# Performance work log

Hardware: AMD Instinct MI355X
Metric: run time of the kernel (lower is better)

The kernel has to match this reference:

```python
import jax, jax.numpy as jnp
import numpy as np

N_HEAD = 8
NORM_GROUPS = 32
EPS = 1e-6


def setup_inputs() -> dict:
    key = jax.random.key(0)
    ks = jax.random.split(key, 9)
    B, C, H, W, D = 1, 256, 16, 16, 16
    COND = 512
    x = jax.random.normal(ks[0], (B, C, H, W, D), dtype=jnp.float32)
    cond = jax.random.normal(ks[1], (B, COND), dtype=jnp.float32)
    # AdaGN linear scale/shift (torch Linear: weight [C, cond_dim], bias [C])
    w_scale = jax.random.normal(ks[2], (C, COND), dtype=jnp.float32) * 0.02
    b_scale = jax.random.normal(ks[3], (C,), dtype=jnp.float32) * 0.02
    w_shift = jax.random.normal(ks[4], (C, COND), dtype=jnp.float32) * 0.02
    b_shift = jax.random.normal(ks[5], (C,), dtype=jnp.float32) * 0.02
    # 1x1x1 conv3d weights collapse to matrices: qkv [3C, C] (no bias), out [C, C] + bias
    w_qkv = jax.random.normal(ks[6], (3 * C, C), dtype=jnp.float32) * (1.0 / np.sqrt(C))
    w_out = jax.random.normal(ks[7], (C, C), dtype=jnp.float32) * (1.0 / np.sqrt(C))
    b_out = jax.random.normal(ks[8], (C,), dtype=jnp.float32) * 0.02
    return {"x": x, "cond": cond, "w_scale": w_scale, "b_scale": b_scale,
            "w_shift": w_shift, "b_shift": b_shift, "w_qkv": w_qkv,
            "w_out": w_out, "b_out": b_out}


def _ada_gn(x, cond, w_scale, b_scale, w_shift, b_shift):
    B, C, H, W, D = x.shape
    G = NORM_GROUPS
    xg = x.reshape(B, G, C // G, H, W, D)
    mean = jnp.mean(xg, axis=(2, 3, 4, 5), keepdims=True)
    var = jnp.var(xg, axis=(2, 3, 4, 5), keepdims=True)
    x_norm = ((xg - mean) * jax.lax.rsqrt(var + EPS)).reshape(B, C, H, W, D)
    scale = (cond @ w_scale.T + b_scale)[:, :, None, None, None]  # [B,C,1,1,1]
    shift = (cond @ w_shift.T + b_shift)[:, :, None, None, None]
    return x_norm * (1.0 + scale) + shift


def reference(x, cond, w_scale, b_scale, w_shift, b_shift, w_qkv, w_out, b_out):
    B, C, H, W, D = x.shape
    nh = N_HEAD
    hd = C // nh
    N = H * W * D  # flattened spatial tokens
    norm = _ada_gn(x, cond, w_scale, b_scale, w_shift, b_shift)
    # 1x1x1 conv == channel matmul
    qkv = jnp.einsum('oc,bchwd->bohwd', w_qkv, norm)        # [B,3C,H,W,D]
    qkv = qkv.reshape(B, nh, 3 * hd, N)
    q, k, v = jnp.split(qkv, 3, axis=2)                      # each [B,nh,hd,N]
    attn = jnp.einsum('bnci,bncj->bnij', q, k) / jnp.sqrt(jnp.float32(C))
    attn = jax.nn.softmax(attn, axis=-1)                     # [B,nh,N,N]
    out = jnp.einsum('bnij,bncj->bnci', attn, v)             # [B,nh,hd,N]
    out = out.reshape(B, C, H, W, D)
    out = jnp.einsum('oc,bchwd->bohwd', w_out, out) + b_out[None, :, None, None, None]
    return out + x
```

## Files before the change

kernel.cpp:

```cpp
#include <hip/hip_runtime.h>
#include <math.h>

#define CCH 256
#define NN  4096
#define NHEAD 8
#define CONDD 512

typedef __attribute__((ext_vector_type(8))) short short8;
typedef __attribute__((ext_vector_type(4))) float f32x4;
typedef __attribute__((ext_vector_type(16))) float f32x16;

static __device__ __forceinline__ short f2bf(float f) {
    union { float f; uint32_t u; } v; v.f = f;
    uint32_t r = v.u + 0x7fffu + ((v.u >> 16) & 1u);
    return (short)(r >> 16);
}

static __device__ __forceinline__ uint32_t cvt_pk_bf16(float a, float b) {
    uint32_t r;
    asm("v_cvt_pk_bf16_f32 %0, %1, %2" : "=v"(r) : "v"(a), "v"(b));
    return r;
}

__global__ __launch_bounds__(256) void front_fused(const float* __restrict__ x,
                                                   const float* __restrict__ cond,
                                                   const float* __restrict__ w_scale,
                                                   const float* __restrict__ b_scale,
                                                   const float* __restrict__ w_shift,
                                                   const float* __restrict__ b_shift,
                                                   const float* __restrict__ wq,
                                                   const float* __restrict__ wo,
                                                   float* __restrict__ partial,
                                                   float* __restrict__ scale,
                                                   float* __restrict__ shift,
                                                   short* __restrict__ wqb,
                                                   short* __restrict__ wob) {
    __shared__ float rs[4], rss[4];
    int bb = blockIdx.x;
    int t = threadIdx.x;
    if (bb < 256) {
        const float4* p = (const float4*)(x + bb * 4096);
        float s = 0.f, ss = 0.f;
        for (int k = t; k < 1024; k += 256) {
            float4 v = p[k];
            s += v.x + v.y + v.z + v.w;
            ss += v.x * v.x + v.y * v.y + v.z * v.z + v.w * v.w;
        }
        #pragma unroll
        for (int off = 32; off; off >>= 1) { s += __shfl_xor(s, off); ss += __shfl_xor(ss, off); }
        int wid = t >> 6;
        if ((t & 63) == 0) { rs[wid] = s; rss[wid] = ss; }
        __syncthreads();
        if (t == 0) {
            partial[2 * bb] = rs[0] + rs[1] + rs[2] + rs[3];
            partial[2 * bb + 1] = rss[0] + rss[1] + rss[2] + rss[3];
        }
    } else if (bb < 1280) {
        int idx = (bb - 256) * 256 + t;
        if (idx < 196608) wqb[idx] = f2bf(wq[idx]);
        else              wob[idx - 196608] = f2bf(wo[idx - 196608]);
    } else {
        int o = (bb - 1280) * 4 + (t >> 6);
        int lane = t & 63;
        float ds = 0.f, dh = 0.f;
        for (int k = lane; k < CONDD; k += 64) {
            float cv = cond[k];
            ds += cv * w_scale[o * CONDD + k];
            dh += cv * w_shift[o * CONDD + k];
        }
        #pragma unroll
        for (int off = 32; off; off >>= 1) { ds += __shfl_xor(ds, off); dh += __shfl_xor(dh, off); }
        if (lane == 0) { scale[o] = ds + b_scale[o]; shift[o] = dh + b_shift[o]; }
    }
}

__global__ __launch_bounds__(256) void normalize_t(const float* __restrict__ x,
                                                   const float* __restrict__ partial,
                                                   const float* __restrict__ scale,
                                                   const float* __restrict__ shift,
                                                   short* __restrict__ norm_t) {
    __shared__ float gm[8], gr[8];
    __shared__ float Aa[64], Bb[64];
    __shared__ short tile[32 * 66];
    int i0 = blockIdx.x * 32;
    int c0 = blockIdx.y * 64;
    int g0 = c0 >> 3;
    int t = threadIdx.x;
    if (t < 8) {
        float s = 0.f, ss = 0.f;
        #pragma unroll
        for (int ch = 0; ch < 8; ++ch) {
            s += partial[((g0 + t) * 8 + ch) * 2];
            ss += partial[((g0 + t) * 8 + ch) * 2 + 1];
        }
        float mean = s * (1.0f / 32768.0f);
        float var = ss * (1.0f / 32768.0f) - mean * mean;
        gm[t] = mean;
        gr[t] = rsqrtf(var + 1e-6f);
    }
    __syncthreads();
    if (t < 64) {
        int c = c0 + t;
        float a = gr[t >> 3] * (1.0f + scale[c]);
        Aa[t] = a;
        Bb[t] = shift[c] - gm[t >> 3] * a;
    }
    __syncthreads();
    #pragma unroll
    for (int e0 = 0; e0 < 8; ++e0) {
        int e = e0 * 256 + t;
        int cl = e >> 5, il = e & 31;
        float v = x[(c0 + cl) * NN + i0 + il];
        tile[il * 66 + cl] = f2bf(v * Aa[cl] + Bb[cl]);
    }
    __syncthreads();
    #pragma unroll
    for (int e0 = 0; e0 < 4; ++e0) {
        int e = e0 * 256 + t;
        int il = e >> 5, cd = e & 31;
        uint32_t d = *(const uint32_t*)&tile[il * 66 + 2 * cd];
        *(uint32_t*)&norm_t[(i0 + il) * 256 + c0 + 2 * cd] = d;
    }
}

__global__ __launch_bounds__(256) void qkv_gemm(const short* __restrict__ wqb,
                                                const short* __restrict__ norm_t,
                                                short* __restrict__ qtb, short* __restrict__ ktb,
                                                short* __restrict__ vcb) {
    int t = threadIdx.x;
    int w = t >> 6, lane = t & 63, li = lane & 15, lg = lane >> 4;
    int o0 = blockIdx.x * 32;
    int i0 = blockIdx.y * 64 + w * 16;
    f32x4 acc[2] = {{0,0,0,0},{0,0,0,0}};
    const short* bbase = norm_t + (i0 + li) * 256 + 8 * lg;
    const short* abase = wqb + (o0 + li) * 256 + 8 * lg;
    #pragma unroll
    for (int ks = 0; ks < 8; ++ks) {
        short8 bfrag = *(const short8*)(bbase + ks * 32);
        #pragma unroll
        for (int f = 0; f < 2; ++f) {
            short8 afrag = *(const short8*)(abase + f * 16 * 256 + ks * 32);
            acc[f] = __builtin_amdgcn_mfma_f32_16x16x32_bf16(afrag, bfrag, acc[f], 0, 0, 0);
        }
    }
    int i = i0 + li;
    #pragma unroll
    for (int f = 0; f < 2; ++f) {
        #pragma unroll
        for (int r = 0; r < 4; ++r) {
            int o = o0 + 16 * f + 4 * lg + r;
            float v = acc[f][r];
            int h = o / 96;
            int rr = o - h * 96;
            int cc = rr & 31;
            int kind = rr >> 5;
            if (kind == 0)      qtb[(h * NN + i) * 32 + cc] = f2bf(v * (0.0625f * 1.44269504f));
            else if (kind == 1) ktb[(h * NN + i) * 32 + cc] = f2bf(v);
            else                vcb[(h * 32 + cc) * NN + i] = f2bf(v);
        }
    }
}

__global__ __launch_bounds__(512, 4) void attention_mfma(const short* __restrict__ qtb,
                                                         const short* __restrict__ ktb,
                                                         const short* __restrict__ vcb,
                                                         short* __restrict__ attnP,
                                                         float* __restrict__ plsum) {
    __shared__ __align__(16) char lds[65536];

    int bid = blockIdx.x;
    int h = bid & 7;
    int qb = (bid >> 3) & 15;
    int kh = bid >> 7;
    int t = threadIdx.x;
    int w = t >> 6, lane = t & 63, l31 = lane & 31, hi = lane >> 5;

    int qbase = qb * 256 + w * 32;
    const short* qrow = qtb + (h * NN + qbase + l31) * 32;
    short8 qf0 = *(const short8*)(qrow + 8 * hi);
    short8 qf1 = *(const short8*)(qrow + 16 + 8 * hi);
    asm volatile("s_waitcnt vmcnt(0)" ::: "memory");

    const char* src0;
    const char* src1;
    int ldsoff0, ldsoff1, step;
    if (w < 4) {
        int row_l = lane >> 2, g_lds = lane & 3;
        int g_glob = g_lds ^ (row_l & 3);
        const char* kbase = (const char*)ktb + (size_t)(h * NN + kh * 1024) * 64;
        int s0 = 2 * w, s1 = 2 * w + 1;
        src0 = kbase + ((s0 >> 2) * 64 + (s0 & 3) * 16 + row_l) * 64 + g_glob * 16;
        src1 = kbase + ((s1 >> 2) * 64 + (s1 & 3) * 16 + row_l) * 64 + g_glob * 16;
        ldsoff0 = s0 * 1024;
        ldsoff1 = s1 * 1024;
        step = 8192;
    } else {
        int row_l = lane >> 3, vs_lds = lane & 7;
        int vg = vs_lds ^ row_l;
        const char* vbase = (const char*)vcb + (size_t)(h * 32) * (NN * 2) + kh * 2048;
        int s0 = 2 * (w - 4), s1 = 2 * (w - 4) + 1;
        src0 = vbase + (size_t)((s0 & 3) * 8 + row_l) * (NN * 2) + (s0 >> 2) * 128 + vg * 16;
        src1 = vbase + (size_t)((s1 & 3) * 8 + row_l) * (NN * 2) + (s1 >> 2) * 128 + vg * 16;
        ldsoff0 = 8192 + s0 * 1024;
        ldsoff1 = 8192 + s1 * 1024;
        step = 256;
    }

    f32x16 acc = {0,0,0,0,0,0,0,0,0,0,0,0,0,0,0,0};
    const f32x16 zero16 = {0,0,0,0,0,0,0,0,0,0,0,0,0,0,0,0};
    float lsum = 0.f;

    #define ISSUE(st, b) do { \
        __builtin_amdgcn_global_load_lds((const uint32_t*)(src0 + (st) * step), \
            (uint32_t*)(lds + (b) * 16384 + ldsoff0), 16, 0, 0); \
        __builtin_amdgcn_global_load_lds((const uint32_t*)(src1 + (st) * step), \
            (uint32_t*)(lds + (b) * 16384 + ldsoff1), 16, 0, 0); \
    } while (0)

    #define COMPUTE(b) do { \
        const char* bb_ = lds + (b) * 16384; \
        _Pragma("unroll") \
        for (int chunk = 0; chunk < 2; ++chunk) { \
            _Pragma("unroll") \
            for (int half = 0; half < 2; ++half) { \
                int jl = half * 32; \
                int R = jl + l31; \
                int rx = R & 3; \
                const char* kr = bb_ + chunk * 4096 + R * 64; \
                short8 kf0 = *(const short8*)(kr + (((hi) ^ rx) << 4)); \
                short8 kf1 = *(const short8*)(kr + (((2 + hi) ^ rx) << 4)); \
                const char* vr = bb_ + 8192 + chunk * 4096 + l31 * 128; \
                int cx = l31 & 7; \
                int sv = (jl >> 3) + hi; \
                short8 vf0 = *(const short8*)(vr + ((sv ^ cx) << 4)); \
                short8 vf1 = *(const short8*)(vr + (((sv + 2) ^ cx) << 4)); \
                __builtin_amdgcn_s_setprio(1); \
                f32x16 s = __builtin_amdgcn_mfma_f32_32x32x16_bf16(kf0, qf0, zero16, 0, 0, 0); \
                s = __builtin_amdgcn_mfma_f32_32x32x16_bf16(kf1, qf1, s, 0, 0, 0); \
                __builtin_amdgcn_s_setprio(0); \
                float p[16]; \
                _Pragma("unroll") \
                for (int r = 0; r < 16; ++r) p[r] = __builtin_amdgcn_exp2f(s[r]); \
                float u0 = 0.f, u1 = 0.f; \
                _Pragma("unroll") \
                for (int r = 0; r < 4; ++r) { u0 += p[r] + p[4 + r]; u1 += p[8 + r] + p[12 + r]; } \
                lsum += u0 + u1; \
                auto A1 = __builtin_amdgcn_permlane32_swap(cvt_pk_bf16(p[0], p[1]),   cvt_pk_bf16(p[4], p[5]),   false, false); \
                auto A2 = __builtin_amdgcn_permlane32_swap(cvt_pk_bf16(p[2], p[3]),   cvt_pk_bf16(p[6], p[7]),   false, false); \
                auto A3 = __builtin_amdgcn_permlane32_swap(cvt_pk_bf16(p[8], p[9]),   cvt_pk_bf16(p[12], p[13]), false, false); \
                auto A4 = __builtin_amdgcn_permlane32_swap(cvt_pk_bf16(p[10], p[11]), cvt_pk_bf16(p[14], p[15]), false, false); \
                union PF { uint32_t u[4]; short8 s8; }; \
                PF f1, f2; \
                f1.u[0] = A1[0]; f1.u[1] = A2[0]; f1.u[2] = A1[1]; f1.u[3] = A2[1]; \
                f2.u[0] = A3[0]; f2.u[1] = A4[0]; f2.u[2] = A3[1]; f2.u[3] = A4[1]; \
                __builtin_amdgcn_s_setprio(1); \
                acc = __builtin_amdgcn_mfma_f32_32x32x16_bf16(vf0, f1.s8, acc, 0, 0, 0); \
                acc = __builtin_amdgcn_mfma_f32_32x32x16_bf16(vf1, f2.s8, acc, 0, 0, 0); \
                __builtin_amdgcn_s_setprio(0); \
            } \
        } \
    } while (0)

    #define WAITV(n) do { \
        asm volatile("s_waitcnt vmcnt(" #n ")" ::: "memory"); \
        __builtin_amdgcn_sched_barrier(0); \
        __builtin_amdgcn_s_barrier(); \
    } while (0)

    ISSUE(0, 0);
    ISSUE(1, 1);
    ISSUE(2, 2);
    WAITV(4);

    ISSUE(3, 3); COMPUTE(0); WAITV(4);
    ISSUE(4, 0); COMPUTE(1); WAITV(4);
    ISSUE(5, 1); COMPUTE(2); WAITV(4);
    ISSUE(6, 2); COMPUTE(3); WAITV(4);
    ISSUE(7, 3); COMPUTE(0); WAITV(4);
    COMPUTE(1); WAITV(2);
    COMPUTE(2); WAITV(0);
    COMPUTE(3);

    #undef ISSUE
    #undef COMPUTE
    #undef WAITV

    __builtin_amdgcn_s_barrier();

    lsum += __shfl_xor(lsum, 32);

    short* tile = (short*)lds + w * 1024;
    #pragma unroll
    for (int g = 0; g < 4; ++g) {
        uint2 u;
        u.x = cvt_pk_bf16(acc[4 * g + 0], acc[4 * g + 1]);
        u.y = cvt_pk_bf16(acc[4 * g + 2], acc[4 * g + 3]);
        *(uint2*)(tile + l31 * 32 + 8 * g + 4 * hi) = u;
    }
    {
        int row = l31, half = hi;
        const uint4* srcp = (const uint4*)(tile + row * 32 + half * 16);
        short* dst = attnP + (size_t)(qbase + row) * 1024 + kh * 256 + h * 32 + half * 16;
        uint4 d0 = srcp[0];
        uint4 d1 = srcp[1];
        *(uint4*)dst = d0;
        *(uint4*)(dst + 8) = d1;
    }
    if (hi == 0) plsum[(size_t)(kh * 8 + h) * NN + qbase + l31] = lsum;
}

__global__ __launch_bounds__(256) void proj_gemm(const short* __restrict__ wob,
                                                 const short* __restrict__ attnP,
                                                 const float* __restrict__ plsum,
                                                 const float* __restrict__ b_out,
                                                 const float* __restrict__ x,
                                                 float* __restrict__ out) {
    __shared__ float invl[8][64];
    int t = threadIdx.x;
    int w = t >> 6, lane = t & 63, li = lane & 15, lg = lane >> 4;
    int o0 = blockIdx.x * 32;
    int i0b = blockIdx.y * 64;
    int i0 = i0b + w * 16;
    {
        int hh = t >> 5, ii = (t & 31) * 2;
        float a = 0.f, b = 0.f;
        #pragma unroll
        for (int kh = 0; kh < 4; ++kh) {
            const float* pl = plsum + (size_t)(kh * 8 + hh) * NN + i0b;
            a += pl[ii];
            b += pl[ii + 1];
        }
        invl[hh][ii] = 1.0f / a;
        invl[hh][ii + 1] = 1.0f / b;
    }
    __syncthreads();
    const short* bbase = attnP + (size_t)(i0 + li) * 1024 + 8 * lg;
    const short* abase = wob + (o0 + li) * 256 + 8 * lg;
    f32x4 facc0 = {0, 0, 0, 0}, facc1 = {0, 0, 0, 0};
    #pragma unroll
    for (int h = 0; h < 8; ++h) {
        short8 af0 = *(const short8*)(abase + h * 32);
        short8 af1 = *(const short8*)(abase + 16 * 256 + h * 32);
        f32x4 acc0 = {0, 0, 0, 0}, acc1 = {0, 0, 0, 0};
        #pragma unroll
        for (int kh = 0; kh < 4; ++kh) {
            short8 bf = *(const short8*)(bbase + kh * 256 + h * 32);
            acc0 = __builtin_amdgcn_mfma_f32_16x16x32_bf16(af0, bf, acc0, 0, 0, 0);
            acc1 = __builtin_amdgcn_mfma_f32_16x16x32_bf16(af1, bf, acc1, 0, 0, 0);
        }
        float iv = invl[h][w * 16 + li];
        facc0 += acc0 * iv;
        facc1 += acc1 * iv;
    }
    int i = i0 + li;
    #pragma unroll
    for (int r = 0; r < 4; ++r) {
        int o = o0 + 4 * lg + r;
        out[o * NN + i] = facc0[r] + b_out[o] + x[o * NN + i];
        int o2 = o0 + 16 + 4 * lg + r;
        out[o2 * NN + i] = facc1[r] + b_out[o2] + x[o2 * NN + i];
    }
}

extern "C" void kernel_launch(void* const* d_in, const int* in_sizes, int n_in,
                              void* d_out, int out_size, void* d_ws, size_t ws_size,
                              hipStream_t stream) {
    const float* x       = (const float*)d_in[0];
    const float* cond    = (const float*)d_in[1];
    const float* w_scale = (const float*)d_in[2];
    const float* b_scale = (const float*)d_in[3];
    const float* w_shift = (const float*)d_in[4];
    const float* b_shift = (const float*)d_in[5];
    const float* w_qkv   = (const float*)d_in[6];
    const float* w_out   = (const float*)d_in[7];
    const float* b_out   = (const float*)d_in[8];
    float* out = (float*)d_out;

    float* ws = (float*)d_ws;
    float* scale   = ws;
    float* shift   = ws + 256;
    float* partial = ws + 512;
    short* norm_t = (short*)(ws + 1024);
    short* qtb = norm_t + 1048576;
    short* ktb = qtb + 1048576;
    short* vcb = ktb + 1048576;
    short* wqb = vcb + 1048576;
    short* wob = wqb + 196608;
    short* attnP = wob + 65536;
    float* plsum = (float*)(attnP + (size_t)4096 * 1024);

    front_fused<<<1344, 256, 0, stream>>>(x, cond, w_scale, b_scale, w_shift, b_shift,
                                          w_qkv, w_out, partial, scale, shift, wqb, wob);
    normalize_t<<<dim3(128, 4), 256, 0, stream>>>(x, partial, scale, shift, norm_t);
    qkv_gemm<<<dim3(24, 64), 256, 0, stream>>>(wqb, norm_t, qtb, ktb, vcb);
    attention_mfma<<<512, 512, 0, stream>>>(qtb, ktb, vcb, attnP, plsum);
    proj_gemm<<<dim3(8, 64), 256, 0, stream>>>(wob, attnP, plsum, b_out, x, out);
}
```

Baseline: 73.69 us.

## Fuse AdaGN normalize into QKV GEMM via swizzled LDS tile

Merges the normalize/transpose kernel into the QKV GEMM. Each block now normalizes a 64-token by 256-channel slab of x straight into a bank-swizzled shared-memory tile and reads its B fragments from there. Output tiles grow from 32 to 128 rows, so there are fewer blocks. This removes one launch and the norm_t round trip through global memory. In exchange, x is re-read and re-normalized by each of the 6 output-column blocks, and the grid shrinks to 384 blocks, which may lower occupancy and parallelism.

After: 79.33 us. 7.7% more time.

```diff
diff --git a/kernel.cpp b/kernel.cpp
--- a/kernel.cpp
+++ b/kernel.cpp
@@ -74,78 +74,72 @@
     }
 }
 
-__global__ __launch_bounds__(256) void normalize_t(const float* __restrict__ x,
-                                                   const float* __restrict__ partial,
-                                                   const float* __restrict__ scale,
-                                                   const float* __restrict__ shift,
-                                                   short* __restrict__ norm_t) {
-    __shared__ float gm[8], gr[8];
-    __shared__ float Aa[64], Bb[64];
-    __shared__ short tile[32 * 66];
-    int i0 = blockIdx.x * 32;
-    int c0 = blockIdx.y * 64;
-    int g0 = c0 >> 3;
+__global__ __launch_bounds__(256, 4) void qkv_fused(const float* __restrict__ x,
+                                                    const float* __restrict__ partial,
+                                                    const float* __restrict__ scale,
+                                                    const float* __restrict__ shift,
+                                                    const short* __restrict__ wqb,
+                                                    short* __restrict__ qtb, short* __restrict__ ktb,
+                                                    short* __restrict__ vcb) {
+    __shared__ float Af[256], Bf[256];
+    __shared__ __align__(16) short nt[16384];
+
     int t = threadIdx.x;
-    if (t < 8) {
+    int o0 = blockIdx.x * 128;
+    int i0 = blockIdx.y * 64;
+
+    {
+        int c = t;
+        int g = c >> 3;
         float s = 0.f, ss = 0.f;
         #pragma unroll
         for (int ch = 0; ch < 8; ++ch) {
-            s += partial[((g0 + t) * 8 + ch) * 2];
-            ss += partial[((g0 + t) * 8 + ch) * 2 + 1];
+            s += partial[(g * 8 + ch) * 2];
+            ss += partial[(g * 8 + ch) * 2 + 1];
         }
         float mean = s * (1.0f / 32768.0f);
         float var = ss * (1.0f / 32768.0f) - mean * mean;
-        gm[t] = mean;
-        gr[t] = rsqrtf(var + 1e-6f);
+        float rstd = rsqrtf(var + 1e-6f);
+        float a = rstd * (1.0f + scale[c]);
+        Af[c] = a;
+        Bf[c] = shift[c] - mean * a;
     }
     __syncthreads();
-    if (t < 64) {
-        int c = c0 + t;
-        float a = gr[t >> 3] * (1.0f + scale[c]);
-        Aa[t] = a;
-        Bb[t] = shift[c] - gm[t >> 3] * a;
+
+    #pragma unroll
+    for (int e = 0; e < 64; ++e) {
+        int lin = e * 256 + t;
+        int cl = lin >> 6;
+        int il = lin & 63;
+        float v = x[cl * NN + i0 + il];
+        float nv = v * Af[cl] + Bf[cl];
+        int slot = cl >> 3;
+        int sw = slot ^ ((il & 7) << 2);
+        *(short*)((char*)nt + il * 512 + sw * 16 + (cl & 7) * 2) = f2bf(nv);
     }
     __syncthreads();
-    #pragma unroll
-    for (int e0 = 0; e0 < 8; ++e0) {
-        int e = e0 * 256 + t;
-        int cl = e >> 5, il = e & 31;
-        float v = x[(c0 + cl) * NN + i0 + il];
-        tile[il * 66 + cl] = f2bf(v * Aa[cl] + Bb[cl]);
-    }
-    __syncthreads();
-    #pragma unroll
-    for (int e0 = 0; e0 < 4; ++e0) {
-        int e = e0 * 256 + t;
-        int il = e >> 5, cd = e & 31;
-        uint32_t d = *(const uint32_t*)&tile[il * 66 + 2 * cd];
-        *(uint32_t*)&norm_t[(i0 + il) * 256 + c0 + 2 * cd] = d;
-    }
-}
-
-__global__ __launch_bounds__(256) void qkv_gemm(const short* __restrict__ wqb,
-                                                const short* __restrict__ norm_t,
-                                                short* __restrict__ qtb, short* __restrict__ ktb,
-                                                short* __restrict__ vcb) {
-    int t = threadIdx.x;
+
     int w = t >> 6, lane = t & 63, li = lane & 15, lg = lane >> 4;
-    int o0 = blockIdx.x * 32;
-    int i0 = blockIdx.y * 64 + w * 16;
-    f32x4 acc[2] = {{0,0,0,0},{0,0,0,0}};
-    const short* bbase = norm_t + (i0 + li) * 256 + 8 * lg;
+    int irow = w * 16 + li;
+
+    f32x4 acc[8] = {{0,0,0,0},{0,0,0,0},{0,0,0,0},{0,0,0,0},
+                    {0,0,0,0},{0,0,0,0},{0,0,0,0},{0,0,0,0}};
     const short* abase = wqb + (o0 + li) * 256 + 8 * lg;
+    const char* brow = (const char*)nt + irow * 512;
+    int swx = (li & 7) << 2;
     #pragma unroll
     for (int ks = 0; ks < 8; ++ks) {
-        short8 bfrag = *(const short8*)(bbase + ks * 32);
-        #pragma unroll
-        for (int f = 0; f < 2; ++f) {
+        int slot = ks * 4 + lg;
+        short8 bfrag = *(const short8*)(brow + (slot ^ swx) * 16);
+        #pragma unroll
+        for (int f = 0; f < 8; ++f) {
             short8 afrag = *(const short8*)(abase + f * 16 * 256 + ks * 32);
             acc[f] = __builtin_amdgcn_mfma_f32_16x16x32_bf16(afrag, bfrag, acc[f], 0, 0, 0);
         }
     }
-    int i = i0 + li;
-    #pragma unroll
-    for (int f = 0; f < 2; ++f) {
+    int i = i0 + irow;
+    #pragma unroll
+    for (int f = 0; f < 8; ++f) {
         #pragma unroll
         for (int r = 0; r < 4; ++r) {
             int o = o0 + 16 * f + 4 * lg + r;
@@ -380,8 +374,7 @@
     float* scale   = ws;
     float* shift   = ws + 256;
     float* partial = ws + 512;
-    short* norm_t = (short*)(ws + 1024);
-    short* qtb = norm_t + 1048576;
+    short* qtb = (short*)(ws + 1024);
     short* ktb = qtb + 1048576;
     short* vcb = ktb + 1048576;
     short* wqb = vcb + 1048576;
@@ -391,8 +384,7 @@
 
     front_fused<<<1344, 256, 0, stream>>>(x, cond, w_scale, b_scale, w_shift, b_shift,
                                           w_qkv, w_out, partial, scale, shift, wqb, wob);
-    normalize_t<<<dim3(128, 4), 256, 0, stream>>>(x, partial, scale, shift, norm_t);
-    qkv_gemm<<<dim3(24, 64), 256, 0, stream>>>(wqb, norm_t, qtb, ktb, vcb);
+    qkv_fused<<<dim3(6, 64), 256, 0, stream>>>(x, partial, scale, shift, wqb, qtb, ktb, vcb);
     attention_mfma<<<512, 512, 0, stream>>>(qtb, ktb, vcb, attnP, plsum);
     proj_gemm<<<dim3(8, 64), 256, 0, stream>>>(wob, attnP, plsum, b_out, x, out);
 }
```
